# Kernel optimization log

Hardware: AMD Instinct MI355X
Metric: run time of the kernel (lower is better)

The kernel has to match this reference:

```python
import jax, jax.numpy as jnp
import numpy as np

N, E = 50000, 800000
IN_DIM, OUT_DIM, H = 256, 128, 8
GEO_HID = 16  # RBF feature dim and geo_mlp hidden dim


def setup_inputs() -> dict:
    key = jax.random.key(0)
    ks = jax.random.split(key, 16)
    def lin(k, fan_out, fan_in):
        kw, kb = jax.random.split(k)
        lim = 1.0 / np.sqrt(fan_in)
        W = jax.random.uniform(kw, (fan_out, fan_in), jnp.float32, -lim, lim)
        b = jax.random.uniform(kb, (fan_out,), jnp.float32, -lim, lim)
        return W, b
    Wq, bq = lin(ks[0], OUT_DIM, IN_DIM)
    Wk, bk = lin(ks[1], OUT_DIM, IN_DIM)
    Wv, bv = lin(ks[2], OUT_DIM, IN_DIM)
    Wo, bo = lin(ks[3], OUT_DIM, OUT_DIM)
    Wg1, bg1 = lin(ks[4], GEO_HID, GEO_HID)
    Wg2, bg2 = lin(ks[5], H, GEO_HID)
    x = jax.random.normal(ks[6], (N, IN_DIM), jnp.float32)
    edge_index = jax.random.randint(ks[7], (2, E), 0, N, jnp.int64)
    edge_dist = jax.random.uniform(ks[8], (E,), jnp.float32) * 6.0
    return {"x": x, "edge_index": edge_index, "edge_dist": edge_dist,
            "Wq": Wq, "bq": bq, "Wk": Wk, "bk": bk, "Wv": Wv, "bv": bv,
            "Wo": Wo, "bo": bo, "Wg1": Wg1, "bg1": bg1, "Wg2": Wg2, "bg2": bg2}


def reference(x, edge_index, edge_dist, Wq, bq, Wk, bk, Wv, bv, Wo, bo, Wg1, bg1, Wg2, bg2):
    n = x.shape[0]
    num_heads = Wg2.shape[0]
    head_dim = Wq.shape[0] // num_heads
    scale = 1.0 / (head_dim ** 0.5)

    q = (x @ Wq.T + bq).reshape(n, num_heads, head_dim)
    k = (x @ Wk.T + bk).reshape(n, num_heads, head_dim)
    v = (x @ Wv.T + bv).reshape(n, num_heads, head_dim)

    # RBF expansion: 16 centers in [0, 6], gamma = 1.0
    centers = jnp.linspace(0.0, 6.0, GEO_HID)
    rbf = jnp.exp(-(edge_dist[:, None] - centers) ** 2)          # [E, 16]
    geo_bias = jax.nn.relu(rbf @ Wg1.T + bg1) @ Wg2.T + bg2      # [E, H]

    row, col = edge_index[0], edge_index[1]
    attn = (q[row] * k[col]).sum(-1) * scale + geo_bias          # [E, H]

    # segment softmax over incoming edges per destination node (row)
    m = jax.ops.segment_max(attn, row, num_segments=n)           # [N, H]
    e = jnp.exp(attn - m[row])
    s = jax.ops.segment_sum(e, row, num_segments=n)              # [N, H]
    a = e / (s[row] + 1e-12)                                     # [E, H]

    out = jax.ops.segment_sum(v[col] * a[:, :, None], row, num_segments=n)
    out = out.reshape(n, num_heads * head_dim)
    return out @ Wo.T + bo
```

## Files before the change

### kernel.cpp

```cpp
#include <hip/hip_runtime.h>
#include <math.h>

#define IN_DIM 256
#define OUT_DIM 128
#define NH 8
#define HD 16
#define GH 16
#define TBL 1024
#define LOG2E 1.44269504f
#define RCAP 64
#define BINSH 6
#define BCAP 1408

typedef __attribute__((ext_vector_type(8))) short short8;
typedef __attribute__((ext_vector_type(4))) float floatx4;

__device__ __forceinline__ unsigned short f2bf(float f) {
    union { float f; unsigned u; } v; v.f = f;
    unsigned r = v.u + 0x7fffu + ((v.u >> 16) & 1u);
    return (unsigned short)(r >> 16);
}
__device__ __forceinline__ float bf2f(unsigned short h) {
    union { unsigned u; float f; } v; v.u = ((unsigned)h) << 16;
    return v.f;
}
__device__ __forceinline__ void split1(float f, unsigned short& h, unsigned short& l) {
    h = f2bf(f);
    l = f2bf(f - bf2f(h));
}
__device__ __forceinline__ float bflo(unsigned u) { return __uint_as_float(u << 16); }
__device__ __forceinline__ float bfhi(unsigned u) { return __uint_as_float(u & 0xffff0000u); }

__global__ __launch_bounds__(256) void prep_all_kernel(
    const float* __restrict__ Wq, const float* __restrict__ Wk,
    const float* __restrict__ Wv, const float* __restrict__ Wo,
    unsigned short* __restrict__ wh, unsigned short* __restrict__ wl,
    unsigned short* __restrict__ wo_h, unsigned short* __restrict__ wo_l,
    const float* __restrict__ Wg1, const float* __restrict__ bg1,
    const float* __restrict__ Wg2, const float* __restrict__ bg2,
    float* __restrict__ tbl, int* __restrict__ gbin,
    int nbins, int nwm, int nwo, int ngeo) {
    int bx = blockIdx.x;
    int t = threadIdx.x;

    if (bx < 3 * nwm) {
        int m = bx / nwm;
        int i = (bx - m * nwm) * 256 + t;
        if (i >= (OUT_DIM * IN_DIM) / 4) return;
        const float* W = (m == 0) ? Wq : (m == 1) ? Wk : Wv;
        float4 f = ((const float4*)W)[i];
        ushort4 h, l;
        split1(f.x, h.x, l.x); split1(f.y, h.y, l.y);
        split1(f.z, h.z, l.z); split1(f.w, h.w, l.w);
        size_t base = (size_t)m * (OUT_DIM * IN_DIM) / 4;
        ((ushort4*)wh)[base + i] = h;
        ((ushort4*)wl)[base + i] = l;
        return;
    }
    bx -= 3 * nwm;
    if (bx < nwo) {
        int i = bx * 256 + t;
        if (i >= (OUT_DIM * OUT_DIM) / 4) return;
        float4 f = ((const float4*)Wo)[i];
        ushort4 h, l;
        split1(f.x, h.x, l.x); split1(f.y, h.y, l.y);
        split1(f.z, h.z, l.z); split1(f.w, h.w, l.w);
        ((ushort4*)wo_h)[i] = h;
        ((ushort4*)wo_l)[i] = l;
        return;
    }
    bx -= nwo;
    if (bx < ngeo) {
        int i = bx * 256 + t;
        if (i >= TBL) return;
        float d = (float)i * (6.0f / (float)(TBL - 1));
        float rbf[GH];
#pragma unroll
        for (int j = 0; j < GH; ++j) {
            float c = 0.4f * (float)j;
            float tt = d - c;
            rbf[j] = __expf(-tt * tt);
        }
        float hid[GH];
#pragma unroll
        for (int j = 0; j < GH; ++j) {
            float acc = bg1[j];
#pragma unroll
            for (int kk = 0; kk < GH; ++kk) acc += rbf[kk] * Wg1[j * GH + kk];
            hid[j] = fmaxf(acc, 0.0f);
        }
#pragma unroll
        for (int h = 0; h < NH; ++h) {
            float acc = bg2[h];
#pragma unroll
            for (int j = 0; j < GH; ++j) acc += hid[j] * Wg2[h * GH + j];
            tbl[i * NH + h] = acc * LOG2E;
        }
        return;
    }
    for (int i = t; i < nbins; i += 256) gbin[i] = 0;
}

__global__ __launch_bounds__(512, 4) void qkv_kernel(
    const float* __restrict__ x,
    const unsigned short* __restrict__ wh, const unsigned short* __restrict__ wl,
    const float* __restrict__ bq, const float* __restrict__ bk, const float* __restrict__ bv,
    float* __restrict__ q, unsigned short* __restrict__ kb, unsigned short* __restrict__ vb,
    const int* __restrict__ ei, const float* __restrict__ edist,
    int* __restrict__ gbin, int2* __restrict__ binbuf,
    int Nn, int E_, int nxb, int nb1, int nbins) {
    __shared__ unsigned short xh_s[128 * 40];
    __shared__ unsigned short xl_s[128 * 40];
    __shared__ unsigned short wh_s[128 * 40];
    __shared__ unsigned short wl_s[128 * 40];

    const int tid = threadIdx.x;
    int bx = blockIdx.x;

    if (bx < nb1) {
        int* hist = (int*)xh_s;
        const int e0 = bx * 4096;
        for (int b = tid; b < nbins; b += 512) hist[b] = 0;
        __syncthreads();
#pragma unroll
        for (int i = 0; i < 8; ++i) {
            int e = e0 + tid + i * 512;
            if (e < E_) atomicAdd(&hist[ei[e] >> BINSH], 1);
        }
        __syncthreads();
        for (int b = tid; b < nbins; b += 512) {
            int h = hist[b];
            int base = 0;
            if (h) base = atomicAdd(&gbin[b], h);
            hist[b] = base;
        }
        __syncthreads();
#pragma unroll
        for (int i = 0; i < 8; ++i) {
            int e = e0 + tid + i * 512;
            if (e < E_) {
                int row = ei[e];
                int bin = row >> BINSH;
                int r = atomicAdd(&hist[bin], 1);
                float u = edist[e] * ((float)(TBL - 1) / 6.0f);
                u = fminf(fmaxf(u, 0.0f), (float)(TBL - 1));
                if (r < BCAP)
                    binbuf[(size_t)bin * BCAP + r] =
                        make_int2((ei[E_ + e] & 0x1FFFF) | ((row & 63) << 17), __float_as_int(u));
            }
        }
        return;
    }
    bx -= nb1;

    const int wsel = bx / nxb;
    const int n0 = (bx - wsel * nxb) * 128;
    const unsigned short* W_h = wh + (size_t)wsel * (OUT_DIM * IN_DIM);
    const unsigned short* W_l = wl + (size_t)wsel * (OUT_DIM * IN_DIM);
    const float* bias = (wsel == 0) ? bq : (wsel == 1) ? bk : bv;
    const bool vpath = (wsel == 2);

    const int w = tid >> 6;
    const int lane = tid & 63;
    const int ml = lane & 15;
    const int quad = lane >> 4;
    const int rg = w & 3;
    const int cg = w >> 2;

    const int rows_valid = min(128, Nn - n0);

    floatx4 acc[2][4];
#pragma unroll
    for (int rr = 0; rr < 2; ++rr)
#pragma unroll
        for (int ct = 0; ct < 4; ++ct) acc[rr][ct] = (floatx4){0.f, 0.f, 0.f, 0.f};

    for (int kc = 0; kc < IN_DIM; kc += 32) {
        {
            int r = tid >> 2, c = tid & 3;
            float xf[8];
            if (r < rows_valid) {
                const float4* xs = (const float4*)(x + (size_t)(n0 + r) * IN_DIM + kc + c * 8);
                float4 a = xs[0], b = xs[1];
                xf[0] = a.x; xf[1] = a.y; xf[2] = a.z; xf[3] = a.w;
                xf[4] = b.x; xf[5] = b.y; xf[6] = b.z; xf[7] = b.w;
            } else {
#pragma unroll
                for (int j = 0; j < 8; ++j) xf[j] = 0.0f;
            }
            size_t gw = (size_t)r * IN_DIM + kc + c * 8;
            if (!vpath) {
                unsigned short hv[8];
#pragma unroll
                for (int j = 0; j < 8; ++j) hv[j] = f2bf(xf[j]);
                *(short8*)(xh_s + r * 40 + c * 8) = *(short8*)hv;
                *(short8*)(wh_s + r * 40 + c * 8) = *(const short8*)(W_h + gw);
            } else {
                unsigned short hv[8], lv[8];
#pragma unroll
                for (int j = 0; j < 8; ++j) split1(xf[j], hv[j], lv[j]);
                *(short8*)(xh_s + r * 40 + c * 8) = *(short8*)hv;
                *(short8*)(xl_s + r * 40 + c * 8) = *(short8*)lv;
                *(short8*)(wh_s + r * 40 + c * 8) = *(const short8*)(W_h + gw);
                *(short8*)(wl_s + r * 40 + c * 8) = *(const short8*)(W_l + gw);
            }
        }
        __syncthreads();

        short8 ah0 = *(const short8*)(xh_s + (rg * 32 + ml) * 40 + quad * 8);
        short8 ah1 = *(const short8*)(xh_s + (rg * 32 + 16 + ml) * 40 + quad * 8);
        if (!vpath) {
#pragma unroll
            for (int ct = 0; ct < 4; ++ct) {
                short8 bh = *(const short8*)(wh_s + (cg * 64 + ct * 16 + ml) * 40 + quad * 8);
                acc[0][ct] = __builtin_amdgcn_mfma_f32_16x16x32_bf16(ah0, bh, acc[0][ct], 0, 0, 0);
                acc[1][ct] = __builtin_amdgcn_mfma_f32_16x16x32_bf16(ah1, bh, acc[1][ct], 0, 0, 0);
            }
        } else {
            short8 al0 = *(const short8*)(xl_s + (rg * 32 + ml) * 40 + quad * 8);
            short8 al1 = *(const short8*)(xl_s + (rg * 32 + 16 + ml) * 40 + quad * 8);
#pragma unroll
            for (int ct = 0; ct < 4; ++ct) {
                short8 bh = *(const short8*)(wh_s + (cg * 64 + ct * 16 + ml) * 40 + quad * 8);
                short8 bl = *(const short8*)(wl_s + (cg * 64 + ct * 16 + ml) * 40 + quad * 8);
                acc[0][ct] = __builtin_amdgcn_mfma_f32_16x16x32_bf16(ah0, bh, acc[0][ct], 0, 0, 0);
                acc[0][ct] = __builtin_amdgcn_mfma_f32_16x16x32_bf16(al0, bh, acc[0][ct], 0, 0, 0);
                acc[0][ct] = __builtin_amdgcn_mfma_f32_16x16x32_bf16(ah0, bl, acc[0][ct], 0, 0, 0);
                acc[1][ct] = __builtin_amdgcn_mfma_f32_16x16x32_bf16(ah1, bh, acc[1][ct], 0, 0, 0);
                acc[1][ct] = __builtin_amdgcn_mfma_f32_16x16x32_bf16(al1, bh, acc[1][ct], 0, 0, 0);
                acc[1][ct] = __builtin_amdgcn_mfma_f32_16x16x32_bf16(ah1, bl, acc[1][ct], 0, 0, 0);
            }
        }
        __syncthreads();
    }

    if (wsel == 0) {
#pragma unroll
        for (int rr = 0; rr < 2; ++rr)
#pragma unroll
            for (int ct = 0; ct < 4; ++ct) {
                int col = cg * 64 + ct * 16 + ml;
                float bj = bias[col];
#pragma unroll
                for (int r = 0; r < 4; ++r) {
                    int grow = n0 + rg * 32 + rr * 16 + quad * 4 + r;
                    if (grow < Nn) q[(size_t)grow * 128 + col] = acc[rr][ct][r] + bj;
                }
            }
    } else {
        unsigned short* ob = (wsel == 1) ? kb : vb;
#pragma unroll
        for (int rr = 0; rr < 2; ++rr)
#pragma unroll
            for (int ct = 0; ct < 4; ++ct) {
                int col = cg * 64 + ct * 16 + ml;
                float bj = bias[col];
#pragma unroll
                for (int r = 0; r < 4; ++r) {
                    int grow = n0 + rg * 32 + rr * 16 + quad * 4 + r;
                    if (grow < Nn) ob[(size_t)grow * 128 + col] = f2bf(acc[rr][ct][r] + bj);
                }
            }
    }
}

__global__ __launch_bounds__(256) void bin2bucket_kernel(
    const int2* __restrict__ binbuf, const int* __restrict__ gbin,
    int2* __restrict__ bucket, int2* __restrict__ meta, int Nn) {
    __shared__ int rcnt[64];
    __shared__ int pref[64];
    __shared__ int2 ebuf[BCAP];
    const int bin = blockIdx.x;
    const int t = threadIdx.x;
    if (t < 64) rcnt[t] = 0;
    __syncthreads();
    int nb = gbin[bin];
    if (nb > BCAP) nb = BCAP;
    const int row0 = bin << BINSH;

    int px[6], py[6], rk[6];
#pragma unroll
    for (int j = 0; j < 6; ++j) {
        int i = t + j * 256;
        rk[j] = -1;
        if (i < nb) {
            int2 p = binbuf[(size_t)bin * BCAP + i];
            int rowrel = (p.x >> 17) & 63;
            int r = atomicAdd(&rcnt[rowrel], 1);
            if (r < RCAP) { px[j] = p.x & 0x1FFFF; py[j] = p.y; rk[j] = r | (rowrel << 16); }
        }
    }
    __syncthreads();
    int myclamp = 0;
    if (t < 64) { myclamp = min(rcnt[t], RCAP); pref[t] = myclamp; }
    __syncthreads();
    for (int off = 1; off < 64; off <<= 1) {
        int v = 0;
        if (t < 64 && t >= off) v = pref[t - off];
        __syncthreads();
        if (t < 64) pref[t] += v;
        __syncthreads();
    }
#pragma unroll
    for (int j = 0; j < 6; ++j) {
        if (rk[j] >= 0) {
            int rowrel = rk[j] >> 16;
            int r = rk[j] & 0xFFFF;
            int pos = pref[rowrel] - min(rcnt[rowrel], RCAP) + r;
            ebuf[pos] = make_int2(px[j], py[j]);
        }
    }
    __syncthreads();
    int total = pref[63];
    const int obase = bin * BCAP;
    for (int i = t; i < total; i += 256) bucket[obase + i] = ebuf[i];
    if (t < 64 && row0 + t < Nn)
        meta[row0 + t] = make_int2(obase + pref[t] - myclamp, myclamp);
}

__global__ __launch_bounds__(256) void fused_node_kernel(
    const float* __restrict__ q, const unsigned short* __restrict__ kb,
    const unsigned short* __restrict__ vb, const int2* __restrict__ bucket,
    const float* __restrict__ tbl, const int2* __restrict__ meta,
    float* __restrict__ o, int Nn) {
    const int lane = threadIdx.x & 63;
    const int g = lane >> 3;
    const int h = lane & 7;
    const int n = blockIdx.x * 4 + (threadIdx.x >> 6);
    if (n >= Nn) return;

    const int2 m = meta[n];
    const int start = m.x;
    const int c = m.y;
    const int end = start + c;

    float qf[16];
    {
        const float4* qp = (const float4*)(q + (size_t)n * 128 + h * 16);
#pragma unroll
        for (int j = 0; j < 4; ++j) {
            float4 t = qp[j];
            qf[j * 4 + 0] = t.x; qf[j * 4 + 1] = t.y;
            qf[j * 4 + 2] = t.z; qf[j * 4 + 3] = t.w;
        }
    }

    float l = 0.0f;
    float acc[16];
#pragma unroll
    for (int j = 0; j < 16; ++j) acc[j] = 0.0f;

    auto edge_math = [&](const uint4& k0, const uint4& k1, const uint4& v0, const uint4& v1,
                         float u, bool valid) {
        unsigned kk[8] = {k0.x, k0.y, k0.z, k0.w, k1.x, k1.y, k1.z, k1.w};
        float d = 0.0f;
#pragma unroll
        for (int j = 0; j < 8; ++j) {
            d = fmaf(bflo(kk[j]), qf[2 * j], d);
            d = fmaf(bfhi(kk[j]), qf[2 * j + 1], d);
        }
        int i0 = min((int)u, TBL - 2);
        float fr = u - (float)i0;
        float t0 = tbl[i0 * NH + h];
        float t1 = tbl[i0 * NH + NH + h];
        float logit2 = fmaf(d, 0.25f * LOG2E, fmaf(fr, t1 - t0, t0));
        logit2 = fminf(logit2, 80.0f);
        if (!valid) logit2 = -1e30f;
        float p = __builtin_amdgcn_exp2f(logit2);
        l += p;
        unsigned vv[8] = {v0.x, v0.y, v0.z, v0.w, v1.x, v1.y, v1.z, v1.w};
#pragma unroll
        for (int j = 0; j < 8; ++j) {
            acc[2 * j]     = fmaf(p, bflo(vv[j]), acc[2 * j]);
            acc[2 * j + 1] = fmaf(p, bfhi(vv[j]), acc[2 * j + 1]);
        }
    };

    if (c > 0) {
        int2 npA = bucket[min(start + g, end - 1)];
        const bool vAv = (start + g < end);
        const bool doB = (end > start + 8);
        int2 npB = npA;
        bool vBv = false;
        if (doB) {
            npB = bucket[min(start + 8 + g, end - 1)];
            vBv = (start + 8 + g < end);
        }
        const uint4* kpA = (const uint4*)(kb + (size_t)npA.x * 128 + h * 16);
        const uint4* vpA = (const uint4*)(vb + (size_t)npA.x * 128 + h * 16);
        uint4 kA0 = kpA[0], kA1 = kpA[1], vA0 = vpA[0], vA1 = vpA[1];
        uint4 kB0, kB1, vB0, vB1;
        if (doB) {
            const uint4* kpB = (const uint4*)(kb + (size_t)npB.x * 128 + h * 16);
            const uint4* vpB = (const uint4*)(vb + (size_t)npB.x * 128 + h * 16);
            kB0 = kpB[0]; kB1 = kpB[1]; vB0 = vpB[0]; vB1 = vpB[1];
        }
        edge_math(kA0, kA1, vA0, vA1, __int_as_float(npA.y), vAv);
        if (doB) edge_math(kB0, kB1, vB0, vB1, __int_as_float(npB.y), vBv);
        for (int base = start + 16; base < end; base += 8) {
            int2 np = bucket[min(base + g, end - 1)];
            bool valid = (base + g < end);
            const uint4* kp = (const uint4*)(kb + (size_t)np.x * 128 + h * 16);
            const uint4* vp = (const uint4*)(vb + (size_t)np.x * 128 + h * 16);
            uint4 k0 = kp[0], k1 = kp[1], v0 = vp[0], v1 = vp[1];
            edge_math(k0, k1, v0, v1, __int_as_float(np.y), valid);
        }
    }

#pragma unroll
    for (int off = 8; off < 64; off <<= 1) {
        l += __shfl_xor(l, off);
#pragma unroll
        for (int j = 0; j < 16; ++j) acc[j] += __shfl_xor(acc[j], off);
    }

    if (g == 0) {
        float inv = 1.0f / (l + 1e-12f);
        float4* op = (float4*)(o + (size_t)n * 128 + h * 16);
#pragma unroll
        for (int j = 0; j < 4; ++j) {
            float4 t;
            t.x = acc[j * 4 + 0] * inv; t.y = acc[j * 4 + 1] * inv;
            t.z = acc[j * 4 + 2] * inv; t.w = acc[j * 4 + 3] * inv;
            op[j] = t;
        }
    }
}

__global__ __launch_bounds__(512, 4) void out_gemm_mfma_kernel(
    const float* __restrict__ o,
    const unsigned short* __restrict__ wo_h, const unsigned short* __restrict__ wo_l,
    const float* __restrict__ bo, float* __restrict__ out, int Nn) {
    const int n0 = blockIdx.x * 128;

    __shared__ unsigned short xh_s[128 * 40];
    __shared__ unsigned short xl_s[128 * 40];
    __shared__ unsigned short wh_s[128 * 40];
    __shared__ unsigned short wl_s[128 * 40];

    const int tid = threadIdx.x;
    const int w = tid >> 6;
    const int lane = tid & 63;
    const int ml = lane & 15;
    const int quad = lane >> 4;
    const int rg = w & 3;
    const int cg = w >> 2;

    const int rows_valid = min(128, Nn - n0);

    floatx4 acc[2][4];
#pragma unroll
    for (int rr = 0; rr < 2; ++rr)
#pragma unroll
        for (int ct = 0; ct < 4; ++ct) acc[rr][ct] = (floatx4){0.f, 0.f, 0.f, 0.f};

    for (int kc = 0; kc < OUT_DIM; kc += 32) {
        {
            int r = tid >> 2, c = tid & 3;
            unsigned short hv[8], lv[8];
            if (r < rows_valid) {
                const float* src = o + (size_t)(n0 + r) * OUT_DIM + kc + c * 8;
#pragma unroll
                for (int j = 0; j < 8; ++j) split1(src[j], hv[j], lv[j]);
            } else {
#pragma unroll
                for (int j = 0; j < 8; ++j) { hv[j] = 0; lv[j] = 0; }
            }
            *(short8*)(xh_s + r * 40 + c * 8) = *(short8*)hv;
            *(short8*)(xl_s + r * 40 + c * 8) = *(short8*)lv;
            size_t gg = (size_t)r * OUT_DIM + kc + c * 8;
            *(short8*)(wh_s + r * 40 + c * 8) = *(const short8*)(wo_h + gg);
            *(short8*)(wl_s + r * 40 + c * 8) = *(const short8*)(wo_l + gg);
        }
        __syncthreads();

        short8 ah0 = *(const short8*)(xh_s + (rg * 32 + ml) * 40 + quad * 8);
        short8 ah1 = *(const short8*)(xh_s + (rg * 32 + 16 + ml) * 40 + quad * 8);
        short8 al0 = *(const short8*)(xl_s + (rg * 32 + ml) * 40 + quad * 8);
        short8 al1 = *(const short8*)(xl_s + (rg * 32 + 16 + ml) * 40 + quad * 8);
#pragma unroll
        for (int ct = 0; ct < 4; ++ct) {
            short8 bh = *(const short8*)(wh_s + (cg * 64 + ct * 16 + ml) * 40 + quad * 8);
            short8 bl = *(const short8*)(wl_s + (cg * 64 + ct * 16 + ml) * 40 + quad * 8);
            acc[0][ct] = __builtin_amdgcn_mfma_f32_16x16x32_bf16(ah0, bh, acc[0][ct], 0, 0, 0);
            acc[0][ct] = __builtin_amdgcn_mfma_f32_16x16x32_bf16(al0, bh, acc[0][ct], 0, 0, 0);
            acc[0][ct] = __builtin_amdgcn_mfma_f32_16x16x32_bf16(ah0, bl, acc[0][ct], 0, 0, 0);
            acc[1][ct] = __builtin_amdgcn_mfma_f32_16x16x32_bf16(ah1, bh, acc[1][ct], 0, 0, 0);
            acc[1][ct] = __builtin_amdgcn_mfma_f32_16x16x32_bf16(al1, bh, acc[1][ct], 0, 0, 0);
            acc[1][ct] = __builtin_amdgcn_mfma_f32_16x16x32_bf16(ah1, bl, acc[1][ct], 0, 0, 0);
        }
        __syncthreads();
    }

#pragma unroll
    for (int rr = 0; rr < 2; ++rr)
#pragma unroll
        for (int ct = 0; ct < 4; ++ct) {
            int col = cg * 64 + ct * 16 + ml;
            float bj = bo[col];
#pragma unroll
            for (int r = 0; r < 4; ++r) {
                int grow = n0 + rg * 32 + rr * 16 + quad * 4 + r;
                if (grow < Nn) out[(size_t)grow * 128 + col] = acc[rr][ct][r] + bj;
            }
        }
}

extern "C" void kernel_launch(void* const* d_in, const int* in_sizes, int n_in,
                              void* d_out, int out_size, void* d_ws, size_t ws_size,
                              hipStream_t stream) {
    const float* x   = (const float*)d_in[0];
    const int* ei    = (const int*)d_in[1];
    const float* edist = (const float*)d_in[2];
    const float* Wq = (const float*)d_in[3];  const float* bq = (const float*)d_in[4];
    const float* Wk = (const float*)d_in[5];  const float* bk = (const float*)d_in[6];
    const float* Wv = (const float*)d_in[7];  const float* bv = (const float*)d_in[8];
    const float* Wo = (const float*)d_in[9];  const float* bo = (const float*)d_in[10];
    const float* Wg1 = (const float*)d_in[11]; const float* bg1 = (const float*)d_in[12];
    const float* Wg2 = (const float*)d_in[13]; const float* bg2 = (const float*)d_in[14];
    const int Nn = in_sizes[0] / IN_DIM;
    const int Ee = in_sizes[2];
    float* out = (float*)d_out;

    char* ws = (char*)d_ws;
    size_t off = 0;
    auto alloc = [&](size_t bytes) -> char* {
        char* p = ws + off;
        off += (bytes + 255) & ~(size_t)255;
        return p;
    };
    float* q  = (float*)alloc((size_t)Nn * 128 * 4);
    unsigned short* kbuf = (unsigned short*)alloc((size_t)Nn * 128 * 2);
    unsigned short* vbuf = (unsigned short*)alloc((size_t)Nn * 128 * 2);
    float* o = (float*)alloc((size_t)Nn * 128 * 4);
    float* geot = (float*)alloc((size_t)TBL * 8 * 4);
    int2* meta = (int2*)alloc((size_t)Nn * 8);
    int nbins = (Nn + 63) >> BINSH;
    int* gbin = (int*)alloc((size_t)nbins * 4);
    unsigned short* wh_all = (unsigned short*)alloc((size_t)3 * OUT_DIM * IN_DIM * 2);
    unsigned short* wl_all = (unsigned short*)alloc((size_t)3 * OUT_DIM * IN_DIM * 2);
    unsigned short* wo_h = (unsigned short*)alloc((size_t)OUT_DIM * OUT_DIM * 2);
    unsigned short* wo_l = (unsigned short*)alloc((size_t)OUT_DIM * OUT_DIM * 2);
    int2* bucket = (int2*)alloc((size_t)nbins * BCAP * 8);

    int2* binbuf = (int2*)o;

    int nwm = ((OUT_DIM * IN_DIM / 4) + 255) / 256;
    int nwo = ((OUT_DIM * OUT_DIM / 4) + 255) / 256;
    int ngeo = (TBL + 255) / 256;
    int gprep = 3 * nwm + nwo + ngeo + 1;
    prep_all_kernel<<<gprep, 256, 0, stream>>>(
        Wq, Wk, Wv, Wo, wh_all, wl_all, wo_h, wo_l,
        Wg1, bg1, Wg2, bg2, geot, gbin, nbins, nwm, nwo, ngeo);

    int nxb = (Nn + 127) / 128;
    int nb1 = (Ee + 4095) / 4096;
    qkv_kernel<<<nb1 + 3 * nxb, 512, 0, stream>>>(
        x, wh_all, wl_all, bq, bk, bv, q, kbuf, vbuf,
        ei, edist, gbin, binbuf, Nn, Ee, nxb, nb1, nbins);

    bin2bucket_kernel<<<nbins, 256, 0, stream>>>(binbuf, gbin, bucket, meta, Nn);

    fused_node_kernel<<<(Nn + 3) / 4, 256, 0, stream>>>(q, kbuf, vbuf, bucket, geot, meta, o, Nn);

    out_gemm_mfma_kernel<<<(Nn + 127) / 128, 512, 0, stream>>>(o, wo_h, wo_l, bo, out, Nn);
}
```

Before: 254.4 us.

## Restructure kernel pipeline: fuse edge scatter with geo table, bucket with QKV GEMM

Reshapes the launch graph. The edge binning scatter now runs in the prep kernel alongside the geo lookup table, with gbin zeroed by a memset. The bin-to-bucket pass is folded into the QKV GEMM launch as extra blocks, so there is one fewer kernel launch and the bucketing overlaps with the GEMM. The separate weight-splitting step is removed, so the GEMM kernels read fp32 weights and convert them to bf16 hi/lo in every block, which adds redundant conversion work and extra weight bandwidth per tile.

Measured after the change: 265.9 us. +4.6%, slower.

```diff
diff --git a/kernel.cpp b/kernel.cpp
--- a/kernel.cpp
+++ b/kernel.cpp
@@ -31,117 +31,40 @@
 __device__ __forceinline__ float bflo(unsigned u) { return __uint_as_float(u << 16); }
 __device__ __forceinline__ float bfhi(unsigned u) { return __uint_as_float(u & 0xffff0000u); }
 
-__global__ __launch_bounds__(256) void prep_all_kernel(
-    const float* __restrict__ Wq, const float* __restrict__ Wk,
-    const float* __restrict__ Wv, const float* __restrict__ Wo,
-    unsigned short* __restrict__ wh, unsigned short* __restrict__ wl,
-    unsigned short* __restrict__ wo_h, unsigned short* __restrict__ wo_l,
+__global__ __launch_bounds__(256) void prep_scatter_kernel(
+    const int* __restrict__ ei, const float* __restrict__ edist,
+    int* __restrict__ gbin, int2* __restrict__ binbuf,
     const float* __restrict__ Wg1, const float* __restrict__ bg1,
     const float* __restrict__ Wg2, const float* __restrict__ bg2,
-    float* __restrict__ tbl, int* __restrict__ gbin,
-    int nbins, int nwm, int nwo, int ngeo) {
+    float* __restrict__ tbl, int E_, int nb1, int nbins) {
+    __shared__ int hist_s[1024];
     int bx = blockIdx.x;
-    int t = threadIdx.x;
-
-    if (bx < 3 * nwm) {
-        int m = bx / nwm;
-        int i = (bx - m * nwm) * 256 + t;
-        if (i >= (OUT_DIM * IN_DIM) / 4) return;
-        const float* W = (m == 0) ? Wq : (m == 1) ? Wk : Wv;
-        float4 f = ((const float4*)W)[i];
-        ushort4 h, l;
-        split1(f.x, h.x, l.x); split1(f.y, h.y, l.y);
-        split1(f.z, h.z, l.z); split1(f.w, h.w, l.w);
-        size_t base = (size_t)m * (OUT_DIM * IN_DIM) / 4;
-        ((ushort4*)wh)[base + i] = h;
-        ((ushort4*)wl)[base + i] = l;
-        return;
-    }
-    bx -= 3 * nwm;
-    if (bx < nwo) {
-        int i = bx * 256 + t;
-        if (i >= (OUT_DIM * OUT_DIM) / 4) return;
-        float4 f = ((const float4*)Wo)[i];
-        ushort4 h, l;
-        split1(f.x, h.x, l.x); split1(f.y, h.y, l.y);
-        split1(f.z, h.z, l.z); split1(f.w, h.w, l.w);
-        ((ushort4*)wo_h)[i] = h;
-        ((ushort4*)wo_l)[i] = l;
-        return;
-    }
-    bx -= nwo;
-    if (bx < ngeo) {
-        int i = bx * 256 + t;
-        if (i >= TBL) return;
-        float d = (float)i * (6.0f / (float)(TBL - 1));
-        float rbf[GH];
-#pragma unroll
-        for (int j = 0; j < GH; ++j) {
-            float c = 0.4f * (float)j;
-            float tt = d - c;
-            rbf[j] = __expf(-tt * tt);
-        }
-        float hid[GH];
-#pragma unroll
-        for (int j = 0; j < GH; ++j) {
-            float acc = bg1[j];
-#pragma unroll
-            for (int kk = 0; kk < GH; ++kk) acc += rbf[kk] * Wg1[j * GH + kk];
-            hid[j] = fmaxf(acc, 0.0f);
-        }
-#pragma unroll
-        for (int h = 0; h < NH; ++h) {
-            float acc = bg2[h];
-#pragma unroll
-            for (int j = 0; j < GH; ++j) acc += hid[j] * Wg2[h * GH + j];
-            tbl[i * NH + h] = acc * LOG2E;
-        }
-        return;
-    }
-    for (int i = t; i < nbins; i += 256) gbin[i] = 0;
-}
-
-__global__ __launch_bounds__(512, 4) void qkv_kernel(
-    const float* __restrict__ x,
-    const unsigned short* __restrict__ wh, const unsigned short* __restrict__ wl,
-    const float* __restrict__ bq, const float* __restrict__ bk, const float* __restrict__ bv,
-    float* __restrict__ q, unsigned short* __restrict__ kb, unsigned short* __restrict__ vb,
-    const int* __restrict__ ei, const float* __restrict__ edist,
-    int* __restrict__ gbin, int2* __restrict__ binbuf,
-    int Nn, int E_, int nxb, int nb1, int nbins) {
-    __shared__ unsigned short xh_s[128 * 40];
-    __shared__ unsigned short xl_s[128 * 40];
-    __shared__ unsigned short wh_s[128 * 40];
-    __shared__ unsigned short wl_s[128 * 40];
-
-    const int tid = threadIdx.x;
-    int bx = blockIdx.x;
+    const int t = threadIdx.x;
 
     if (bx < nb1) {
-        int* hist = (int*)xh_s;
         const int e0 = bx * 4096;
-        for (int b = tid; b < nbins; b += 512) hist[b] = 0;
-        __syncthreads();
-#pragma unroll
-        for (int i = 0; i < 8; ++i) {
-            int e = e0 + tid + i * 512;
-            if (e < E_) atomicAdd(&hist[ei[e] >> BINSH], 1);
-        }
-        __syncthreads();
-        for (int b = tid; b < nbins; b += 512) {
-            int h = hist[b];
+        for (int b = t; b < nbins; b += 256) hist_s[b] = 0;
+        __syncthreads();
+#pragma unroll
+        for (int i = 0; i < 16; ++i) {
+            int e = e0 + t + i * 256;
+            if (e < E_) atomicAdd(&hist_s[ei[e] >> BINSH], 1);
+        }
+        __syncthreads();
+        for (int b = t; b < nbins; b += 256) {
+            int h = hist_s[b];
             int base = 0;
             if (h) base = atomicAdd(&gbin[b], h);
-            hist[b] = base;
-        }
-        __syncthreads();
-#pragma unroll
-        for (int i = 0; i < 8; ++i) {
-            int e = e0 + tid + i * 512;
+            hist_s[b] = base;
+        }
+        __syncthreads();
+#pragma unroll
+        for (int i = 0; i < 16; ++i) {
+            int e = e0 + t + i * 256;
             if (e < E_) {
                 int row = ei[e];
                 int bin = row >> BINSH;
-                int r = atomicAdd(&hist[bin], 1);
+                int r = atomicAdd(&hist_s[bin], 1);
                 float u = edist[e] * ((float)(TBL - 1) / 6.0f);
                 u = fminf(fmaxf(u, 0.0f), (float)(TBL - 1));
                 if (r < BCAP)
@@ -152,11 +75,108 @@
         return;
     }
     bx -= nb1;
+    {
+        int i = bx * 256 + t;
+        if (i >= TBL) return;
+        float d = (float)i * (6.0f / (float)(TBL - 1));
+        float rbf[GH];
+#pragma unroll
+        for (int j = 0; j < GH; ++j) {
+            float c = 0.4f * (float)j;
+            float tt = d - c;
+            rbf[j] = __expf(-tt * tt);
+        }
+        float hid[GH];
+#pragma unroll
+        for (int j = 0; j < GH; ++j) {
+            float acc = bg1[j];
+#pragma unroll
+            for (int kk = 0; kk < GH; ++kk) acc += rbf[kk] * Wg1[j * GH + kk];
+            hid[j] = fmaxf(acc, 0.0f);
+        }
+#pragma unroll
+        for (int h = 0; h < NH; ++h) {
+            float acc = bg2[h];
+#pragma unroll
+            for (int j = 0; j < GH; ++j) acc += hid[j] * Wg2[h * GH + j];
+            tbl[i * NH + h] = acc * LOG2E;
+        }
+    }
+}
+
+__global__ __launch_bounds__(512, 4) void qkv_kernel(
+    const float* __restrict__ x,
+    const float* __restrict__ Wq, const float* __restrict__ Wk, const float* __restrict__ Wv,
+    const float* __restrict__ bq, const float* __restrict__ bk, const float* __restrict__ bv,
+    float* __restrict__ q, unsigned short* __restrict__ kb, unsigned short* __restrict__ vb,
+    const int2* __restrict__ binbuf, const int* __restrict__ gbin,
+    int2* __restrict__ bucket, int2* __restrict__ meta,
+    int Nn, int nxb, int nbins) {
+    __shared__ unsigned short lds_u[4 * 128 * 40];
+
+    const int tid = threadIdx.x;
+    int bx = blockIdx.x;
+
+    if (bx < nbins) {
+        int* rcnt = (int*)lds_u;
+        int* pref = rcnt + 64;
+        int2* ebuf = (int2*)(pref + 64);
+        const int bin = bx;
+        if (tid < 64) rcnt[tid] = 0;
+        __syncthreads();
+        int nb = gbin[bin];
+        if (nb > BCAP) nb = BCAP;
+        const int row0 = bin << BINSH;
+
+        int px[3], py[3], rk[3];
+#pragma unroll
+        for (int j = 0; j < 3; ++j) {
+            int i = tid + j * 512;
+            rk[j] = -1;
+            if (i < nb) {
+                int2 p = binbuf[(size_t)bin * BCAP + i];
+                int rowrel = (p.x >> 17) & 63;
+                int r = atomicAdd(&rcnt[rowrel], 1);
+                if (r < RCAP) { px[j] = p.x & 0x1FFFF; py[j] = p.y; rk[j] = r | (rowrel << 16); }
+            }
+        }
+        __syncthreads();
+        int myclamp = 0;
+        if (tid < 64) { myclamp = min(rcnt[tid], RCAP); pref[tid] = myclamp; }
+        __syncthreads();
+        for (int off = 1; off < 64; off <<= 1) {
+            int v = 0;
+            if (tid < 64 && tid >= off) v = pref[tid - off];
+            __syncthreads();
+            if (tid < 64) pref[tid] += v;
+            __syncthreads();
+        }
+#pragma unroll
+        for (int j = 0; j < 3; ++j) {
+            if (rk[j] >= 0) {
+                int rowrel = rk[j] >> 16;
+                int r = rk[j] & 0xFFFF;
+                ebuf[pref[rowrel] - min(rcnt[rowrel], RCAP) + r] = make_int2(px[j], py[j]);
+            }
+        }
+        __syncthreads();
+        int total = pref[63];
+        const int obase = bin * BCAP;
+        for (int i = tid; i < total; i += 512) bucket[obase + i] = ebuf[i];
+        if (tid < 64 && row0 + tid < Nn)
+            meta[row0 + tid] = make_int2(obase + pref[tid] - myclamp, myclamp);
+        return;
+    }
+    bx -= nbins;
+
+    unsigned short* xh_s = lds_u;
+    unsigned short* xl_s = lds_u + 128 * 40;
+    unsigned short* wh_s = lds_u + 2 * 128 * 40;
+    unsigned short* wl_s = lds_u + 3 * 128 * 40;
 
     const int wsel = bx / nxb;
     const int n0 = (bx - wsel * nxb) * 128;
-    const unsigned short* W_h = wh + (size_t)wsel * (OUT_DIM * IN_DIM);
-    const unsigned short* W_l = wl + (size_t)wsel * (OUT_DIM * IN_DIM);
+    const float* Wf = (wsel == 0) ? Wq : (wsel == 1) ? Wk : Wv;
     const float* bias = (wsel == 0) ? bq : (wsel == 1) ? bk : bv;
     const bool vpath = (wsel == 2);
 
@@ -188,21 +208,27 @@
 #pragma unroll
                 for (int j = 0; j < 8; ++j) xf[j] = 0.0f;
             }
-            size_t gw = (size_t)r * IN_DIM + kc + c * 8;
+            float wf[8];
+            {
+                const float4* wsrc = (const float4*)(Wf + (size_t)r * IN_DIM + kc + c * 8);
+                float4 a = wsrc[0], b = wsrc[1];
+                wf[0] = a.x; wf[1] = a.y; wf[2] = a.z; wf[3] = a.w;
+                wf[4] = b.x; wf[5] = b.y; wf[6] = b.z; wf[7] = b.w;
+            }
             if (!vpath) {
-                unsigned short hv[8];
-#pragma unroll
-                for (int j = 0; j < 8; ++j) hv[j] = f2bf(xf[j]);
+                unsigned short hv[8], wv[8];
+#pragma unroll
+                for (int j = 0; j < 8; ++j) { hv[j] = f2bf(xf[j]); wv[j] = f2bf(wf[j]); }
                 *(short8*)(xh_s + r * 40 + c * 8) = *(short8*)hv;
-                *(short8*)(wh_s + r * 40 + c * 8) = *(const short8*)(W_h + gw);
+                *(short8*)(wh_s + r * 40 + c * 8) = *(short8*)wv;
             } else {
-                unsigned short hv[8], lv[8];
-#pragma unroll
-                for (int j = 0; j < 8; ++j) split1(xf[j], hv[j], lv[j]);
+                unsigned short hv[8], lv[8], wvh[8], wvl[8];
+#pragma unroll
+                for (int j = 0; j < 8; ++j) { split1(xf[j], hv[j], lv[j]); split1(wf[j], wvh[j], wvl[j]); }
                 *(short8*)(xh_s + r * 40 + c * 8) = *(short8*)hv;
                 *(short8*)(xl_s + r * 40 + c * 8) = *(short8*)lv;
-                *(short8*)(wh_s + r * 40 + c * 8) = *(const short8*)(W_h + gw);
-                *(short8*)(wl_s + r * 40 + c * 8) = *(const short8*)(W_l + gw);
+                *(short8*)(wh_s + r * 40 + c * 8) = *(short8*)wvh;
+                *(short8*)(wl_s + r * 40 + c * 8) = *(short8*)wvl;
             }
         }
         __syncthreads();
@@ -242,9 +268,9 @@
                 int col = cg * 64 + ct * 16 + ml;
                 float bj = bias[col];
 #pragma unroll
-                for (int r = 0; r < 4; ++r) {
-                    int grow = n0 + rg * 32 + rr * 16 + quad * 4 + r;
-                    if (grow < Nn) q[(size_t)grow * 128 + col] = acc[rr][ct][r] + bj;
+                for (int rr2 = 0; rr2 < 4; ++rr2) {
+                    int grow = n0 + rg * 32 + rr * 16 + quad * 4 + rr2;
+                    if (grow < Nn) q[(size_t)grow * 128 + col] = acc[rr][ct][rr2] + bj;
                 }
             }
     } else {
@@ -256,66 +282,12 @@
                 int col = cg * 64 + ct * 16 + ml;
                 float bj = bias[col];
 #pragma unroll
-                for (int r = 0; r < 4; ++r) {
-                    int grow = n0 + rg * 32 + rr * 16 + quad * 4 + r;
-                    if (grow < Nn) ob[(size_t)grow * 128 + col] = f2bf(acc[rr][ct][r] + bj);
+                for (int rr2 = 0; rr2 < 4; ++rr2) {
+                    int grow = n0 + rg * 32 + rr * 16 + quad * 4 + rr2;
+                    if (grow < Nn) ob[(size_t)grow * 128 + col] = f2bf(acc[rr][ct][rr2] + bj);
                 }
             }
     }
-}
-
-__global__ __launch_bounds__(256) void bin2bucket_kernel(
-    const int2* __restrict__ binbuf, const int* __restrict__ gbin,
-    int2* __restrict__ bucket, int2* __restrict__ meta, int Nn) {
-    __shared__ int rcnt[64];
-    __shared__ int pref[64];
-    __shared__ int2 ebuf[BCAP];
-    const int bin = blockIdx.x;
-    const int t = threadIdx.x;
-    if (t < 64) rcnt[t] = 0;
-    __syncthreads();
-    int nb = gbin[bin];
-    if (nb > BCAP) nb = BCAP;
-    const int row0 = bin << BINSH;
-
-    int px[6], py[6], rk[6];
-#pragma unroll
-    for (int j = 0; j < 6; ++j) {
-        int i = t + j * 256;
-        rk[j] = -1;
-        if (i < nb) {
-            int2 p = binbuf[(size_t)bin * BCAP + i];
-            int rowrel = (p.x >> 17) & 63;
-            int r = atomicAdd(&rcnt[rowrel], 1);
-            if (r < RCAP) { px[j] = p.x & 0x1FFFF; py[j] = p.y; rk[j] = r | (rowrel << 16); }
-        }
-    }
-    __syncthreads();
-    int myclamp = 0;
-    if (t < 64) { myclamp = min(rcnt[t], RCAP); pref[t] = myclamp; }
-    __syncthreads();
-    for (int off = 1; off < 64; off <<= 1) {
-        int v = 0;
-        if (t < 64 && t >= off) v = pref[t - off];
-        __syncthreads();
-        if (t < 64) pref[t] += v;
-        __syncthreads();
-    }
-#pragma unroll
-    for (int j = 0; j < 6; ++j) {
-        if (rk[j] >= 0) {
-            int rowrel = rk[j] >> 16;
-            int r = rk[j] & 0xFFFF;
-            int pos = pref[rowrel] - min(rcnt[rowrel], RCAP) + r;
-            ebuf[pos] = make_int2(px[j], py[j]);
-        }
-    }
-    __syncthreads();
-    int total = pref[63];
-    const int obase = bin * BCAP;
-    for (int i = t; i < total; i += 256) bucket[obase + i] = ebuf[i];
-    if (t < 64 && row0 + t < Nn)
-        meta[row0 + t] = make_int2(obase + pref[t] - myclamp, myclamp);
 }
 
 __global__ __launch_bounds__(256) void fused_node_kernel(
@@ -428,8 +400,7 @@
 }
 
 __global__ __launch_bounds__(512, 4) void out_gemm_mfma_kernel(
-    const float* __restrict__ o,
-    const unsigned short* __restrict__ wo_h, const unsigned short* __restrict__ wo_l,
+    const float* __restrict__ o, const float* __restrict__ Wo,
     const float* __restrict__ bo, float* __restrict__ out, int Nn) {
     const int n0 = blockIdx.x * 128;
 
@@ -468,9 +439,14 @@
             }
             *(short8*)(xh_s + r * 40 + c * 8) = *(short8*)hv;
             *(short8*)(xl_s + r * 40 + c * 8) = *(short8*)lv;
-            size_t gg = (size_t)r * OUT_DIM + kc + c * 8;
-            *(short8*)(wh_s + r * 40 + c * 8) = *(const short8*)(wo_h + gg);
-            *(short8*)(wl_s + r * 40 + c * 8) = *(const short8*)(wo_l + gg);
+            unsigned short wvh[8], wvl[8];
+            {
+                const float* wsrc = Wo + (size_t)r * OUT_DIM + kc + c * 8;
+#pragma unroll
+                for (int j = 0; j < 8; ++j) split1(wsrc[j], wvh[j], wvl[j]);
+            }
+            *(short8*)(wh_s + r * 40 + c * 8) = *(short8*)wvh;
+            *(short8*)(wl_s + r * 40 + c * 8) = *(short8*)wvl;
         }
         __syncthreads();
 
@@ -499,9 +475,9 @@
             int col = cg * 64 + ct * 16 + ml;
             float bj = bo[col];
 #pragma unroll
-            for (int r = 0; r < 4; ++r) {
-                int grow = n0 + rg * 32 + rr * 16 + quad * 4 + r;
-                if (grow < Nn) out[(size_t)grow * 128 + col] = acc[rr][ct][r] + bj;
+            for (int rr2 = 0; rr2 < 4; ++rr2) {
+                int grow = n0 + rg * 32 + rr * 16 + quad * 4 + rr2;
+                if (grow < Nn) out[(size_t)grow * 128 + col] = acc[rr][ct][rr2] + bj;
             }
         }
 }
@@ -537,31 +513,23 @@
     int2* meta = (int2*)alloc((size_t)Nn * 8);
     int nbins = (Nn + 63) >> BINSH;
     int* gbin = (int*)alloc((size_t)nbins * 4);
-    unsigned short* wh_all = (unsigned short*)alloc((size_t)3 * OUT_DIM * IN_DIM * 2);
-    unsigned short* wl_all = (unsigned short*)alloc((size_t)3 * OUT_DIM * IN_DIM * 2);
-    unsigned short* wo_h = (unsigned short*)alloc((size_t)OUT_DIM * OUT_DIM * 2);
-    unsigned short* wo_l = (unsigned short*)alloc((size_t)OUT_DIM * OUT_DIM * 2);
     int2* bucket = (int2*)alloc((size_t)nbins * BCAP * 8);
 
     int2* binbuf = (int2*)o;
 
-    int nwm = ((OUT_DIM * IN_DIM / 4) + 255) / 256;
-    int nwo = ((OUT_DIM * OUT_DIM / 4) + 255) / 256;
+    hipMemsetAsync(gbin, 0, (size_t)nbins * 4, stream);
+
+    int nb1 = (Ee + 4095) / 4096;
     int ngeo = (TBL + 255) / 256;
-    int gprep = 3 * nwm + nwo + ngeo + 1;
-    prep_all_kernel<<<gprep, 256, 0, stream>>>(
-        Wq, Wk, Wv, Wo, wh_all, wl_all, wo_h, wo_l,
-        Wg1, bg1, Wg2, bg2, geot, gbin, nbins, nwm, nwo, ngeo);
+    prep_scatter_kernel<<<nb1 + ngeo, 256, 0, stream>>>(
+        ei, edist, gbin, binbuf, Wg1, bg1, Wg2, bg2, geot, Ee, nb1, nbins);
 
     int nxb = (Nn + 127) / 128;
-    int nb1 = (Ee + 4095) / 4096;
-    qkv_kernel<<<nb1 + 3 * nxb, 512, 0, stream>>>(
-        x, wh_all, wl_all, bq, bk, bv, q, kbuf, vbuf,
-        ei, edist, gbin, binbuf, Nn, Ee, nxb, nb1, nbins);
-
-    bin2bucket_kernel<<<nbins, 256, 0, stream>>>(binbuf, gbin, bucket, meta, Nn);
+    qkv_kernel<<<nbins + 3 * nxb, 512, 0, stream>>>(
+        x, Wq, Wk, Wv, bq, bk, bv, q, kbuf, vbuf,
+        binbuf, gbin, bucket, meta, Nn, nxb, nbins);
 
     fused_node_kernel<<<(Nn + 3) / 4, 256, 0, stream>>>(q, kbuf, vbuf, bucket, geot, meta, o, Nn);
 
-    out_gemm_mfma_kernel<<<(Nn + 127) / 128, 512, 0, stream>>>(o, wo_h, wo_l, bo, out, Nn);
-}
+    out_gemm_mfma_kernel<<<(Nn + 127) / 128, 512, 0, stream>>>(o, Wo, bo, out, Nn);
+}
```
